# Performance work log

Measured on AMD Instinct MI355X. Metric: run time of the kernel, lower is better.

## Reference

```python
import jax, jax.numpy as jnp
import numpy as np

B, D, S, O = 32768, 1024, 64, 4  # batch, feature_dim, n_subjects, n_outputs


def setup_inputs() -> dict:
    key = jax.random.key(0)
    kx, ks, kw, kb = jax.random.split(key, 4)
    x = jax.random.normal(kx, (B, D), dtype=jnp.float32)          # backbone features
    subject_ids = jax.random.randint(ks, (B,), 0, S)              # per-sample head id
    W = jax.random.normal(kw, (S, D, O), dtype=jnp.float32) / np.float32(np.sqrt(D))
    b = jax.random.normal(kb, (S, O), dtype=jnp.float32) * 0.01
    return {"x": x, "subject_ids": subject_ids, "W": W, "b": b}


def reference(x, subject_ids, W, b):
    # Vectorized form of the per-subject loop:
    #   for sid in unique(subject_ids): outputs[idxs] = heads[sid](features[idxs])
    # Each head is Linear(D, O): out[i] = x[i] @ W[sid[i]] + b[sid[i]].
    Wg = jnp.take(W, subject_ids, axis=0)   # [B, D, O] gathered per-sample weights
    bg = jnp.take(b, subject_ids, axis=0)   # [B, O]
    return jnp.einsum('bd,bdo->bo', x, Wg) + bg
```

## Files before the change

kernel.cpp:

```cpp
#include <hip/hip_runtime.h>

constexpr int B = 32768;
constexpr int D = 1024;
constexpr int S = 64;
constexpr int O = 4;

__global__ __launch_bounds__(256) void tl_heads_kernel(
    const float* __restrict__ x,
    const int*   __restrict__ sid,
    const float* __restrict__ W,
    const float* __restrict__ bias,
    float*       __restrict__ out)
{
    const int gtid = blockIdx.x * blockDim.x + threadIdx.x;
    const int row  = gtid >> 6;
    const int lane = threadIdx.x & 63;
    if (row >= B) return;

    const int s = sid[row];
    const float* __restrict__ xr = x + (size_t)row * D;
    const float* __restrict__ Wr = W + (size_t)s * (D * O);

    float a0 = 0.f, a1 = 0.f, a2 = 0.f, a3 = 0.f;

    #pragma unroll
    for (int k = 0; k < 16; ++k) {
        const int d = k * 64 + lane;
        const float  xv = xr[d];
        const float4 wv = *(const float4*)(Wr + (size_t)d * O);
        a0 += xv * wv.x;
        a1 += xv * wv.y;
        a2 += xv * wv.z;
        a3 += xv * wv.w;
    }

    #pragma unroll
    for (int off = 32; off >= 1; off >>= 1) {
        a0 += __shfl_xor(a0, off, 64);
        a1 += __shfl_xor(a1, off, 64);
        a2 += __shfl_xor(a2, off, 64);
        a3 += __shfl_xor(a3, off, 64);
    }

    if (lane == 0) {
        const float4 bv = *(const float4*)(bias + s * O);
        float4 o4;
        o4.x = a0 + bv.x;
        o4.y = a1 + bv.y;
        o4.z = a2 + bv.z;
        o4.w = a3 + bv.w;
        *(float4*)(out + (size_t)row * O) = o4;
    }
}

extern "C" void kernel_launch(void* const* d_in, const int* in_sizes, int n_in,
                              void* d_out, int out_size, void* d_ws, size_t ws_size,
                              hipStream_t stream) {
    const float* x    = (const float*)d_in[0];
    const int*   sid  = (const int*)d_in[1];
    const float* W    = (const float*)d_in[2];
    const float* bias = (const float*)d_in[3];
    float* out = (float*)d_out;

    const int blocks = B / 4;
    tl_heads_kernel<<<blocks, 256, 0, stream>>>(x, sid, W, bias, out);
}
```

Measured before the change: 205.1 us.

## Bucket rows by subject so each block keeps one head's weights in registers

A single-block counting-sort kernel groups row indices by subject id into the workspace, recording per-subject offsets. The main kernel then launches 16 blocks per subject. Each block stages that subject's weight matrix once into LDS and then registers, and its waves stride over only the rows belonging to that subject, loading x with float4 reads. This removes the per-row re-read of the 16 KB weight slice that the per-row kernel did. In exchange it adds an extra serial launch, scattered row access through the permutation, and load imbalance if subject counts are uneven.

```diff
diff --git a/kernel.cpp b/kernel.cpp
--- a/kernel.cpp
+++ b/kernel.cpp
@@ -5,51 +5,113 @@
 constexpr int S = 64;
 constexpr int O = 4;
 
-__global__ __launch_bounds__(256) void tl_heads_kernel(
-    const float* __restrict__ x,
-    const int*   __restrict__ sid,
-    const float* __restrict__ W,
-    const float* __restrict__ bias,
-    float*       __restrict__ out)
-{
-    const int gtid = blockIdx.x * blockDim.x + threadIdx.x;
-    const int row  = gtid >> 6;
-    const int lane = threadIdx.x & 63;
-    if (row >= B) return;
+constexpr int BLOCKS_PER_SID = 16;
+constexpr int MAIN_BLOCKS    = S * BLOCKS_PER_SID;
+constexpr int WAVES_PER_SID  = BLOCKS_PER_SID * 4;
 
-    const int s = sid[row];
-    const float* __restrict__ xr = x + (size_t)row * D;
-    const float* __restrict__ Wr = W + (size_t)s * (D * O);
+#define WS_OFFSETS 0
+#define WS_PERM    256
 
-    float a0 = 0.f, a1 = 0.f, a2 = 0.f, a3 = 0.f;
+__global__ __launch_bounds__(1024) void sort_kernel(const int* __restrict__ sid,
+                                                    int* __restrict__ ws) {
+    __shared__ int h[S];
+    __shared__ int off[S];
+    const int t = threadIdx.x;
+    if (t < S) h[t] = 0;
+    __syncthreads();
+
+    int myR[B / 1024];
+    int myS[B / 1024];
+    #pragma unroll
+    for (int it = 0; it < B / 1024; ++it) {
+        const int i = it * 1024 + t;
+        const int s = sid[i];
+        myS[it] = s;
+        myR[it] = atomicAdd(&h[s], 1);
+    }
+    __syncthreads();
+
+    if (t == 0) {
+        int acc = 0;
+        for (int s2 = 0; s2 < S; ++s2) {
+            off[s2] = acc;
+            ws[WS_OFFSETS + s2] = acc;
+            acc += h[s2];
+        }
+        ws[WS_OFFSETS + S] = acc;
+    }
+    __syncthreads();
 
     #pragma unroll
-    for (int k = 0; k < 16; ++k) {
-        const int d = k * 64 + lane;
-        const float  xv = xr[d];
-        const float4 wv = *(const float4*)(Wr + (size_t)d * O);
-        a0 += xv * wv.x;
-        a1 += xv * wv.y;
-        a2 += xv * wv.z;
-        a3 += xv * wv.w;
+    for (int it = 0; it < B / 1024; ++it) {
+        const int i = it * 1024 + t;
+        ws[WS_PERM + off[myS[it]] + myR[it]] = i;
     }
+}
 
+__global__ __launch_bounds__(256) void main_kernel(const float* __restrict__ x,
+                                                   const float* __restrict__ W,
+                                                   const float* __restrict__ bias,
+                                                   const int* __restrict__ ws,
+                                                   float* __restrict__ out) {
+    __shared__ float4 Wl[D];
+
+    const int s    = blockIdx.x / BLOCKS_PER_SID;
+    const int blk  = blockIdx.x % BLOCKS_PER_SID;
+    const int wave = threadIdx.x >> 6;
+    const int lane = threadIdx.x & 63;
+
+    const float4* __restrict__ Wg = (const float4*)(W + (size_t)s * (D * O));
+    for (int d = threadIdx.x; d < D; d += 256) Wl[d] = Wg[d];
+    __syncthreads();
+
+    float4 w[4][4];
     #pragma unroll
-    for (int off = 32; off >= 1; off >>= 1) {
-        a0 += __shfl_xor(a0, off, 64);
-        a1 += __shfl_xor(a1, off, 64);
-        a2 += __shfl_xor(a2, off, 64);
-        a3 += __shfl_xor(a3, off, 64);
-    }
+    for (int k = 0; k < 4; ++k)
+        #pragma unroll
+        for (int j = 0; j < 4; ++j)
+            w[k][j] = Wl[k * 256 + lane * 4 + j];
 
-    if (lane == 0) {
-        const float4 bv = *(const float4*)(bias + s * O);
-        float4 o4;
-        o4.x = a0 + bv.x;
-        o4.y = a1 + bv.y;
-        o4.z = a2 + bv.z;
-        o4.w = a3 + bv.w;
-        *(float4*)(out + (size_t)row * O) = o4;
+    const int start = ws[WS_OFFSETS + s];
+    const int cnt   = ws[WS_OFFSETS + s + 1] - start;
+    const int wv_id = blk * 4 + wave;
+
+    const int   q  = (lane >> 2) & 3;
+    const float bb = bias[s * O + q];
+
+    int i   = wv_id;
+    int row = (i < cnt) ? ws[WS_PERM + start + i] : 0;
+    while (i < cnt) {
+        const int i_next   = i + WAVES_PER_SID;
+        const int row_next = (i_next < cnt) ? ws[WS_PERM + start + i_next] : 0;
+
+        const float* __restrict__ xr = x + (size_t)row * D;
+        float a0 = 0.f, a1 = 0.f, a2 = 0.f, a3 = 0.f;
+        #pragma unroll
+        for (int k = 0; k < 4; ++k) {
+            const float4 xv = *(const float4*)(xr + k * 256 + lane * 4);
+            a0 += xv.x * w[k][0].x + xv.y * w[k][1].x + xv.z * w[k][2].x + xv.w * w[k][3].x;
+            a1 += xv.x * w[k][0].y + xv.y * w[k][1].y + xv.z * w[k][2].y + xv.w * w[k][3].y;
+            a2 += xv.x * w[k][0].z + xv.y * w[k][1].z + xv.z * w[k][2].z + xv.w * w[k][3].z;
+            a3 += xv.x * w[k][0].w + xv.y * w[k][1].w + xv.z * w[k][2].w + xv.w * w[k][3].w;
+        }
+
+        #pragma unroll
+        for (int m = 4; m <= 32; m <<= 1) {
+            a0 += __shfl_xor(a0, m, 64);
+            a1 += __shfl_xor(a1, m, 64);
+            a2 += __shfl_xor(a2, m, 64);
+            a3 += __shfl_xor(a3, m, 64);
+        }
+        float v = (q == 0) ? a0 : (q == 1) ? a1 : (q == 2) ? a2 : a3;
+        v += __shfl_xor(v, 1, 64);
+        v += __shfl_xor(v, 2, 64);
+
+        if (lane < 16 && (lane & 3) == 0)
+            out[(size_t)row * O + q] = v + bb;
+
+        i   = i_next;
+        row = row_next;
     }
 }
 
@@ -61,7 +123,8 @@
     const float* W    = (const float*)d_in[2];
     const float* bias = (const float*)d_in[3];
     float* out = (float*)d_out;
+    int* ws = (int*)d_ws;
 
-    const int blocks = B / 4;
-    tl_heads_kernel<<<blocks, 256, 0, stream>>>(x, sid, W, bias, out);
+    sort_kernel<<<1, 1024, 0, stream>>>(sid, ws);
+    main_kernel<<<MAIN_BLOCKS, 256, 0, stream>>>(x, W, bias, ws, out);
 }
```

Result: slower. 222.6 us (+8.6%).

## Persistent waves with register-prefetched rows and a split shuffle reduction

Applied to the files above, without the earlier changes.

The one-wave-per-row launch becomes a persistent grid of 1024 blocks in which each wave walks several rows strided by the total wave count. The next row's x and its W slice are prefetched into registers while the current row's FMAs run, so memory latency overlaps with compute. The reduction is restructured: two xor steps on all four accumulators, then each 16-lane quarter picks one output and reduces it, so four lanes write scalars. This raises register pressure (around 100 VGPRs for prefetch buffers) and lowers the number of waves in flight, trading occupancy for explicit software pipelining of a bandwidth-bound kernel.

```diff
diff --git a/kernel.cpp b/kernel.cpp
--- a/kernel.cpp
+++ b/kernel.cpp
@@ -5,51 +5,92 @@
 constexpr int S = 64;
 constexpr int O = 4;
 
-__global__ __launch_bounds__(256) void tl_heads_kernel(
+constexpr int BLOCKS        = 1024;
+constexpr int WAVES         = BLOCKS * 4;
+constexpr int ROWS_PER_WAVE = B / WAVES;
+
+__global__ __launch_bounds__(256, 4) void main_kernel(
     const float* __restrict__ x,
     const int*   __restrict__ sid,
     const float* __restrict__ W,
     const float* __restrict__ bias,
     float*       __restrict__ out)
 {
-    const int gtid = blockIdx.x * blockDim.x + threadIdx.x;
-    const int row  = gtid >> 6;
     const int lane = threadIdx.x & 63;
-    if (row >= B) return;
+    const int wave = __builtin_amdgcn_readfirstlane(threadIdx.x >> 6);
+    const int w0   = blockIdx.x * 4 + wave;
 
-    const int s = sid[row];
-    const float* __restrict__ xr = x + (size_t)row * D;
-    const float* __restrict__ Wr = W + (size_t)s * (D * O);
+    const int q = lane >> 4;
 
-    float a0 = 0.f, a1 = 0.f, a2 = 0.f, a3 = 0.f;
+    int row = w0;
+    int s   = sid[row];
 
-    #pragma unroll
-    for (int k = 0; k < 16; ++k) {
-        const int d = k * 64 + lane;
-        const float  xv = xr[d];
-        const float4 wv = *(const float4*)(Wr + (size_t)d * O);
-        a0 += xv * wv.x;
-        a1 += xv * wv.y;
-        a2 += xv * wv.z;
-        a3 += xv * wv.w;
+    float xs[16];
+    {
+        const float* __restrict__ xr = x + (size_t)row * D;
+        #pragma unroll
+        for (int k = 0; k < 16; ++k) xs[k] = xr[k * 64 + lane];
+    }
+    float4 wv[16];
+    {
+        const float4* __restrict__ Wr = (const float4*)(W + (size_t)s * (D * O));
+        #pragma unroll
+        for (int k = 0; k < 16; ++k) wv[k] = Wr[k * 64 + lane];
     }
 
-    #pragma unroll
-    for (int off = 32; off >= 1; off >>= 1) {
-        a0 += __shfl_xor(a0, off, 64);
-        a1 += __shfl_xor(a1, off, 64);
-        a2 += __shfl_xor(a2, off, 64);
-        a3 += __shfl_xor(a3, off, 64);
-    }
+    #pragma unroll 1
+    for (int it = 0; it < ROWS_PER_WAVE; ++it) {
+        const bool has_next = (it + 1 < ROWS_PER_WAVE);
+        const int  row_next = row + WAVES;
 
-    if (lane == 0) {
-        const float4 bv = *(const float4*)(bias + s * O);
-        float4 o4;
-        o4.x = a0 + bv.x;
-        o4.y = a1 + bv.y;
-        o4.z = a2 + bv.z;
-        o4.w = a3 + bv.w;
-        *(float4*)(out + (size_t)row * O) = o4;
+        int s_next = 0;
+        if (has_next) s_next = sid[row_next];
+
+        float xn[16];
+        if (has_next) {
+            const float* __restrict__ xrn = x + (size_t)row_next * D;
+            #pragma unroll
+            for (int k = 0; k < 16; ++k) xn[k] = xrn[k * 64 + lane];
+        }
+
+        float a0 = 0.f, a1 = 0.f, a2 = 0.f, a3 = 0.f;
+        #pragma unroll
+        for (int k = 0; k < 16; ++k) {
+            a0 += xs[k] * wv[k].x;
+            a1 += xs[k] * wv[k].y;
+            a2 += xs[k] * wv[k].z;
+            a3 += xs[k] * wv[k].w;
+        }
+
+        if (has_next) {
+            const float4* __restrict__ Wrn = (const float4*)(W + (size_t)s_next * (D * O));
+            #pragma unroll
+            for (int k = 0; k < 16; ++k) wv[k] = Wrn[k * 64 + lane];
+        }
+
+        const float bb = bias[s * O + q];
+
+        #pragma unroll
+        for (int m = 16; m <= 32; m <<= 1) {
+            a0 += __shfl_xor(a0, m, 64);
+            a1 += __shfl_xor(a1, m, 64);
+            a2 += __shfl_xor(a2, m, 64);
+            a3 += __shfl_xor(a3, m, 64);
+        }
+        float v = (q == 0) ? a0 : (q == 1) ? a1 : (q == 2) ? a2 : a3;
+        #pragma unroll
+        for (int m = 1; m <= 8; m <<= 1)
+            v += __shfl_xor(v, m, 64);
+
+        if ((lane & 15) == 0)
+            out[(size_t)row * O + q] = v + bb;
+
+        if (has_next) {
+            #pragma unroll
+            for (int k = 0; k < 16; ++k) xs[k] = xn[k];
+            row = row_next;
+            s   = s_next;
+        }
     }
 }
 
@@ -62,6 +103,5 @@
     const float* bias = (const float*)d_in[3];
     float* out = (float*)d_out;
 
-    const int blocks = B / 4;
-    tl_heads_kernel<<<blocks, 256, 0, stream>>>(x, sid, W, bias, out);
+    main_kernel<<<BLOCKS, 256, 0, stream>>>(x, sid, W, bias, out);
 }
```

Result: slower. 417.6 us (+103.7%).
